# Performance work log

Measured on AMD Instinct MI355X. Metric: run time of the kernel, lower is better.

The kernel has to match this reference:

```python
import jax, jax.numpy as jnp
import numpy as np

ATTN_DIM = 1024
LATENT_DIM = 1024
N_HEADS = 16
HEAD_SIZE = ATTN_DIM // N_HEADS


def setup_inputs() -> dict:
    key = jax.random.key(0)
    ks = jax.random.split(key, 7)
    B, T = 2, 2048
    s_in = 1.0 / np.sqrt(LATENT_DIM)
    s_a = 1.0 / np.sqrt(ATTN_DIM)
    return {
        "x": jax.random.normal(ks[0], (B, T, LATENT_DIM), jnp.float32),
        "w_attn": jax.random.normal(ks[1], (LATENT_DIM, ATTN_DIM), jnp.float32) * s_in,
        "b_attn": jnp.zeros((ATTN_DIM,), jnp.float32),
        "w_qkv": jax.random.normal(ks[2], (ATTN_DIM, 3 * ATTN_DIM), jnp.float32) * s_a,
        "b_qkv": jnp.zeros((3 * ATTN_DIM,), jnp.float32),
        "w_proj": jax.random.normal(ks[3], (ATTN_DIM, ATTN_DIM), jnp.float32) * s_a,
        "b_proj": jnp.zeros((ATTN_DIM,), jnp.float32),
    }


def reference(x, w_attn, b_attn, w_qkv, b_qkv, w_proj, b_proj):
    # x: [B, T, latent_dim]
    h = jnp.einsum("btl,lc->btc", x, w_attn) + b_attn  # [B,T,C]
    B, T, C = h.shape
    qkv = jnp.einsum("btc,cd->btd", h, w_qkv) + b_qkv  # [B,T,3C]
    q, k, v = jnp.split(qkv, 3, axis=2)
    def heads(t):  # [B,T,C] -> [B,H,T,hs]
        return t.reshape(B, T, N_HEADS, HEAD_SIZE).transpose(0, 2, 1, 3)
    q, k, v = heads(q), heads(k), heads(v)
    scale = 1.0 / np.sqrt(HEAD_SIZE)
    scores = jnp.einsum("bhqd,bhkd->bhqk", q, k) * scale  # [B,H,T,T]
    attn = jax.nn.softmax(scores, axis=-1)
    out = jnp.einsum("bhqk,bhkd->bhqd", attn, v)  # [B,H,T,hs]
    out = out.transpose(0, 2, 1, 3).reshape(B, T, C)
    return jnp.einsum("btc,cd->btd", out, w_proj) + b_proj
```

## Files before the change

kernel.cpp:

```cpp
#include <hip/hip_runtime.h>

typedef unsigned short u16;
typedef unsigned int u32;
typedef __bf16 bf16x8 __attribute__((ext_vector_type(8)));
typedef float f32x4 __attribute__((ext_vector_type(4)));
typedef float f32x16 __attribute__((ext_vector_type(16)));
typedef unsigned uint2v __attribute__((ext_vector_type(2)));

typedef const __attribute__((address_space(1))) void* gcp_t;
typedef __attribute__((address_space(3))) void* lp_t;
#define GLDS16(g, l) __builtin_amdgcn_global_load_lds((gcp_t)(g), (lp_t)(l), 16, 0, 0)

__device__ __forceinline__ u16 f2bf(float f) {
  unsigned int u = __builtin_bit_cast(unsigned int, f);
  u += 0x7fffu + ((u >> 16) & 1u);
  return (u16)(u >> 16);
}
__device__ __forceinline__ u16 bfc(float f) {
  return __builtin_bit_cast(u16, (__bf16)f);
}
__device__ __forceinline__ u32 pkbf(float lo, float hi) {
  return (u32)bfc(lo) | ((u32)bfc(hi) << 16);
}
__device__ __forceinline__ float ex2(float x) {
  return __builtin_amdgcn_exp2f(x);
}

__global__ __launch_bounds__(256) void prep(const float* __restrict__ x, u16* __restrict__ xb,
                                            const float* __restrict__ wa, u16* __restrict__ wTa,
                                            const float* __restrict__ wq, u16* __restrict__ wTq,
                                            const float* __restrict__ wp, u16* __restrict__ wTp) {
  __shared__ float tile[32][33];
  const int idx = (int)blockIdx.x;
  const int tid = (int)threadIdx.x;
  if (idx < 2048) {
    long i = ((long)idx * 256 + tid) * 8;
    float4 a = *(const float4*)(x + i);
    float4 b = *(const float4*)(x + i + 4);
    union { u16 u[8]; int4 v; } pk;
    pk.u[0] = f2bf(a.x); pk.u[1] = f2bf(a.y); pk.u[2] = f2bf(a.z); pk.u[3] = f2bf(a.w);
    pk.u[4] = f2bf(b.x); pk.u[5] = f2bf(b.y); pk.u[6] = f2bf(b.z); pk.u[7] = f2bf(b.w);
    *(int4*)(xb + i) = pk.v;
    return;
  }
  const float* in; u16* out; int K, N, bx, by;
  if (idx < 3072) {
    int id = idx - 2048; in = wa; out = wTa; K = 1024; N = 1024; bx = id & 31; by = id >> 5;
  } else if (idx < 6144) {
    int id = idx - 3072; in = wq; out = wTq; K = 1024; N = 3072; bx = id % 96; by = id / 96;
  } else {
    int id = idx - 6144; in = wp; out = wTp; K = 1024; N = 1024; bx = id & 31; by = id >> 5;
  }
  const int n0 = bx * 32, k0 = by * 32;
  const int tx = tid & 31, ty = tid >> 5;
#pragma unroll
  for (int i = 0; i < 4; ++i)
    tile[ty + i * 8][tx] = in[(long)(k0 + ty + i * 8) * N + n0 + tx];
  __syncthreads();
#pragma unroll
  for (int i = 0; i < 4; ++i)
    out[(long)(n0 + ty + i * 8) * K + k0 + tx] = f2bf(tile[tx][ty + i * 8]);
}

template <int BM, int BN, int WN_WAVES, typename OutT, bool VSPLIT = false>
__global__ __launch_bounds__(256) void gemm_bt(const u16* __restrict__ A,
                                               const u16* __restrict__ Bt,
                                               const float* __restrict__ bias,
                                               OutT* __restrict__ C,
                                               u16* __restrict__ vout,
                                               int M, int N, int K) {
  constexpr int WM = BM / (4 / WN_WAVES);
  constexpr int WN = BN / WN_WAVES;
  constexpr int MF = WM / 16, NF = WN / 16;
  constexpr int STG = 2 * BM * 32 + 2 * BN * 32;
  constexpr int TRN = VSPLIT ? 128 * 136 : 0;
  constexpr int CEP = (sizeof(OutT) == 2) ? (BM * BN) : (2 * BM * BN);
  constexpr int PS1 = STG > TRN ? STG : TRN;
  constexpr int PSZ = PS1 > CEP ? PS1 : CEP;
  __shared__ __align__(16) u16 pool[PSZ];
  u16* lA0 = pool;
  u16* lB0 = pool + 2 * BM * 32;
  const int tid = (int)threadIdx.x;
  const int ln = tid & 63;
  const int w = tid >> 6;
  const int wr = w / WN_WAVES, wc = w % WN_WAVES;
  const int lr = ln & 15, lg = ln >> 4;

  const int nwg = (int)(gridDim.x * gridDim.y);
  const int lin = (int)(blockIdx.y * gridDim.x + blockIdx.x);
  const int cpx = nwg >> 3;
  const int swzb = (lin & 7) * cpx + (lin >> 3);
  const int bx = swzb % (int)gridDim.x;
  const int by = swzb / (int)gridDim.x;
  const long mBase = (long)by * BM;
  const long nBase = (long)bx * BN;

  f32x4 acc[MF][NF] = {};

  const int r0 = ln >> 2;
  const int c0 = (ln & 3) * 8;

  auto stage = [&](int buf, int k0) {
#pragma unroll
    for (int i = 0; i < BM / 64; ++i) {
      const int br = (i * 4 + w) * 16;
      GLDS16(A + (mBase + br + r0) * K + k0 + c0, lA0 + buf * BM * 32 + br * 32);
    }
#pragma unroll
    for (int i = 0; i < BN / 64; ++i) {
      const int br = (i * 4 + w) * 16;
      GLDS16(Bt + (nBase + br + r0) * K + k0 + c0, lB0 + buf * BN * 32 + br * 32);
    }
  };

  stage(0, 0);
  __syncthreads();
  int cur = 0;
  for (int k0 = 0; k0 < K; k0 += 32) {
    if (k0 + 32 < K) stage(cur ^ 1, k0 + 32);
    bf16x8 af[MF], bfv[NF];
#pragma unroll
    for (int mi = 0; mi < MF; ++mi)
      af[mi] = *(const bf16x8*)&lA0[cur * BM * 32 + (wr * WM + mi * 16 + lr) * 32 + lg * 8];
#pragma unroll
    for (int ni = 0; ni < NF; ++ni)
      bfv[ni] = *(const bf16x8*)&lB0[cur * BN * 32 + (wc * WN + ni * 16 + lr) * 32 + lg * 8];
#pragma unroll
    for (int mi = 0; mi < MF; ++mi)
#pragma unroll
      for (int ni = 0; ni < NF; ++ni)
        acc[mi][ni] = __builtin_amdgcn_mfma_f32_16x16x32_bf16(af[mi], bfv[ni],
                                                              acc[mi][ni], 0, 0, 0);
    __syncthreads();
    cur ^= 1;
  }

  if (VSPLIT && nBase >= 2048) {
#pragma unroll
    for (int ni = 0; ni < NF; ++ni) {
      const int cl = wc * WN + ni * 16 + lr;
      const float bv = bias ? bias[nBase + cl] : 0.f;
#pragma unroll
      for (int mi = 0; mi < MF; ++mi) {
#pragma unroll
        for (int j = 0; j < 4; ++j) {
          const int rl = wr * WM + mi * 16 + lg * 4 + j;
          pool[cl * 136 + rl] = bfc(acc[mi][ni][j] + bv);
        }
      }
    }
    __syncthreads();
    const int c = tid >> 1, half = tid & 1;
    const long cglob = nBase + c - 2048;
    const int hh2 = (int)(cglob >> 6), d = (int)(cglob & 63);
    const int bb = (int)(mBase >> 11);
    const int t0 = (int)(mBase & 2047);
    u16* dst = vout + ((long)(bb * 16 + hh2) * 64 + d) * 2048 + t0 + half * 64;
    const u16* srcp = &pool[c * 136 + half * 64];
#pragma unroll
    for (int i = 0; i < 8; ++i)
      *(int4*)(dst + i * 8) = *(const int4*)(srcp + i * 8);
    return;
  }

  if constexpr (sizeof(OutT) == 2) {
#pragma unroll
    for (int ni = 0; ni < NF; ++ni) {
      const int col = wc * WN + ni * 16 + lr;
      const float bv = bias ? bias[nBase + col] : 0.f;
#pragma unroll
      for (int mi = 0; mi < MF; ++mi)
#pragma unroll
        for (int j = 0; j < 4; ++j)
          pool[(wr * WM + mi * 16 + lg * 4 + j) * BN + col] = bfc(acc[mi][ni][j] + bv);
    }
    __syncthreads();
    constexpr int SL = BN / 8;
#pragma unroll
    for (int it = 0; it < BM * SL / 256; ++it) {
      const int S = it * 256 + tid;
      const int row = S / SL, si = S % SL;
      *(int4*)&C[(mBase + row) * N + nBase + si * 8] =
          *(const int4*)&pool[row * BN + si * 8];
    }
  } else {
    float* pf = (float*)pool;
#pragma unroll
    for (int ni = 0; ni < NF; ++ni) {
      const int col = wc * WN + ni * 16 + lr;
      const float bv = bias ? bias[nBase + col] : 0.f;
#pragma unroll
      for (int mi = 0; mi < MF; ++mi)
#pragma unroll
        for (int j = 0; j < 4; ++j)
          pf[(wr * WM + mi * 16 + lg * 4 + j) * BN + col] = acc[mi][ni][j] + bv;
    }
    __syncthreads();
    constexpr int SLF = BN / 4;
#pragma unroll
    for (int it = 0; it < BM * SLF / 256; ++it) {
      const int S = it * 256 + tid;
      const int row = S / SLF, si = S % SLF;
      *(f32x4*)&C[(mBase + row) * N + nBase + si * 4] =
          *(const f32x4*)&pf[row * BN + si * 4];
    }
  }
}

__global__ __launch_bounds__(512, 4) void attn_fwd(const u16* __restrict__ qkv,
                                                   const u16* __restrict__ vt,
                                                   u16* __restrict__ outp) {
  __shared__ __align__(16) u16 smem[2][2][2][64 * 64];
  const int tid = (int)threadIdx.x;
  const int ln = tid & 63;
  const int l31 = tid & 31;
  const int hiH = (tid >> 5) & 1;
  const int w = tid >> 6;
  const int g = w >> 2;
  const int qw = w & 3;
  const int bid0 = (int)blockIdx.x;
  const int bid = ((bid0 & 7) << 6) | (bid0 >> 3);
  const int qt = bid & 15;
  const int bh = bid >> 4;
  const int b = bh >> 4;
  const int hh = bh & 15;

  const float SCALE = 0.125f * 1.44269504088896f;

  const long qrow = (long)(b * 2048 + qt * 128 + qw * 32 + l31);
  const u16* Qp = qkv + qrow * 3072 + hh * 64;
  bf16x8 qf[4];
#pragma unroll
  for (int ks = 0; ks < 4; ++ks) {
    union { u16 u[8]; int4 i4; bf16x8 v; } in, ov;
    in.i4 = *(const int4*)(Qp + ks * 16 + hiH * 8);
#pragma unroll
    for (int e = 0; e < 8; ++e) {
      float f = __builtin_bit_cast(float, (u32)in.u[e] << 16) * SCALE;
      ov.u[e] = f2bf(f);
    }
    qf[ks] = ov.v;
  }

  f32x16 o[2] = {};
  float lsum = 0.f;

  const u16* Kbase = qkv + ((long)b * 2048) * 3072 + 1024 + hh * 64;
  const u16* Vbase = vt + (long)bh * 64 * 2048;

  const int sr = ln >> 3;
  const int scm = ln & 7;

  auto stageKV = [&](int buf, int t) {
    const int kv0 = (g * 16 + t) * 64;
#pragma unroll
    for (int i = 0; i < 2; ++i) {
      const int br = (i * 4 + qw) * 8;
      const int r = br + sr;
      const int cs = scm ^ (r & 7);
      GLDS16(Kbase + (long)(kv0 + r) * 3072 + cs * 8, &smem[g][buf][0][br * 64]);
      GLDS16(Vbase + (long)r * 2048 + kv0 + cs * 8, &smem[g][buf][1][br * 64]);
    }
  };

  stageKV(0, 0);
  __syncthreads();
  int cur = 0;
  for (int kt = 0; kt < 16; ++kt) {
    if (kt + 1 < 16) stageKV(cur ^ 1, kt + 1);
    const char* lK = (const char*)&smem[g][cur][0][0];
    const char* lV = (const char*)&smem[g][cur][1][0];

    f32x16 st[2] = {};
#pragma unroll
    for (int t = 0; t < 2; ++t) {
#pragma unroll
      for (int ks = 0; ks < 4; ++ks) {
        const int r = t * 32 + l31;
        int off = (r * 64 + ks * 16 + hiH * 8) * 2;
        off ^= (r & 7) << 4;
        const bf16x8 kf = *(const bf16x8*)(lK + off);
        st[t] = __builtin_amdgcn_mfma_f32_32x32x16_bf16(kf, qf[ks], st[t], 0, 0, 0);
      }
    }

#pragma unroll
    for (int t = 0; t < 2; ++t)
#pragma unroll
      for (int r = 0; r < 16; ++r) st[t][r] = ex2(st[t][r]);
    float ts[16];
#pragma unroll
    for (int r = 0; r < 16; ++r) ts[r] = st[0][r] + st[1][r];
#pragma unroll
    for (int s = 8; s > 0; s >>= 1)
#pragma unroll
      for (int r = 0; r < 8; ++r)
        if (r < s) ts[r] += ts[r + s];
    lsum += ts[0];

    bf16x8 pa[4];
#pragma unroll
    for (int t = 0; t < 2; ++t) {
#pragma unroll
      for (int gg = 0; gg < 2; ++gg) {
        const int bse = gg * 8;
        u32 A = pkbf(st[t][bse + 0], st[t][bse + 1]);
        u32 B = pkbf(st[t][bse + 2], st[t][bse + 3]);
        u32 C = pkbf(st[t][bse + 4], st[t][bse + 5]);
        u32 D = pkbf(st[t][bse + 6], st[t][bse + 7]);
        union { u32 wv[4]; bf16x8 v; } u;
#if __has_builtin(__builtin_amdgcn_permlane32_swap)
        uint2v r0 = __builtin_amdgcn_permlane32_swap(A, C, false, false);
        uint2v r1 = __builtin_amdgcn_permlane32_swap(B, D, false, false);
        u.wv[0] = r0[0]; u.wv[1] = r1[0]; u.wv[2] = r0[1]; u.wv[3] = r1[1];
#else
        const u32 sA = __shfl_xor((int)A, 32);
        const u32 sB = __shfl_xor((int)B, 32);
        const u32 sC = __shfl_xor((int)C, 32);
        const u32 sD = __shfl_xor((int)D, 32);
        u.wv[0] = hiH ? sC : A;
        u.wv[1] = hiH ? sD : B;
        u.wv[2] = hiH ? C : sA;
        u.wv[3] = hiH ? D : sB;
#endif
        pa[t * 2 + gg] = u.v;
      }
    }

#pragma unroll
    for (int dt = 0; dt < 2; ++dt) {
#pragma unroll
      for (int ks2 = 0; ks2 < 4; ++ks2) {
        const int r = dt * 32 + l31;
        int off = (r * 64 + ks2 * 16 + hiH * 8) * 2;
        off ^= (r & 7) << 4;
        const bf16x8 vf = *(const bf16x8*)(lV + off);
        o[dt] = __builtin_amdgcn_mfma_f32_32x32x16_bf16(vf, pa[ks2], o[dt], 0, 0, 0);
      }
    }
    __syncthreads();
    cur ^= 1;
  }

  const float lsum_tot = lsum + __shfl_xor(lsum, 32);
  float* PO = (float*)&smem[0][0][0][0];
  float* MLf = (float*)((char*)PO + 32768);

  if (g == 1) {
    float* dst = PO + (w - 4) * 2048 + ln * 32;
#pragma unroll
    for (int dt = 0; dt < 2; ++dt)
#pragma unroll
      for (int q4 = 0; q4 < 4; ++q4) {
        f32x4 c;
#pragma unroll
        for (int j = 0; j < 4; ++j) c[j] = o[dt][q4 * 4 + j];
        *(f32x4*)(dst + dt * 16 + q4 * 4) = c;
      }
    MLf[(w - 4) * 64 + ln] = lsum_tot;
  }
  __syncthreads();
  if (g == 0) {
    const float l1 = MLf[w * 64 + ln];
    const float* src = PO + w * 2048 + ln * 32;
    const float linv = 1.0f / (lsum_tot + l1);
    u16* T = (u16*)((char*)smem + 36864) + w * (32 * 72);
#pragma unroll
    for (int dt = 0; dt < 2; ++dt) {
      float o1[16];
#pragma unroll
      for (int q4 = 0; q4 < 4; ++q4) {
        const f32x4 c = *(const f32x4*)(src + dt * 16 + q4 * 4);
#pragma unroll
        for (int j = 0; j < 4; ++j) o1[q4 * 4 + j] = c[j];
      }
#pragma unroll
      for (int r = 0; r < 16; ++r) {
        const float v = (o[dt][r] + o1[r]) * linv;
        const int d = (r & 3) + 8 * (r >> 2) + 4 * hiH + dt * 32;
        T[l31 * 72 + d] = bfc(v);
      }
    }
    asm volatile("s_waitcnt lgkmcnt(0)" ::: "memory");
    __builtin_amdgcn_sched_barrier(0);
    const int rr = ln >> 1;
    const int c0 = (ln & 1) * 32;
    u16* orow = outp + ((long)(b * 2048 + qt * 128 + w * 32 + rr)) * 1024 + hh * 64 + c0;
#pragma unroll
    for (int i = 0; i < 4; ++i)
      *(int4*)(orow + i * 8) = *(const int4*)&T[rr * 72 + c0 + i * 8];
  }
}

extern "C" void kernel_launch(void* const* d_in, const int* in_sizes, int n_in,
                              void* d_out, int out_size, void* d_ws, size_t ws_size,
                              hipStream_t stream) {
  (void)in_sizes; (void)n_in; (void)out_size;
  const float* x = (const float*)d_in[0];
  const float* b_attn = (const float*)d_in[2];
  const float* b_qkv = (const float*)d_in[4];
  const float* b_proj = (const float*)d_in[6];

  char* ws = (char*)d_ws;
  const size_t MB = 1024 * 1024;
  u16* xb   = (u16*)(ws + 0 * MB);
  u16* hbuf = (u16*)(ws + 8 * MB);
  u16* qkvb = (u16*)(ws + 16 * MB);
  u16* vtb  = (u16*)(ws + 40 * MB);
  u16* aout = (u16*)(ws + 48 * MB);
  u16* wTa  = (u16*)(ws + 56 * MB);
  u16* wTq  = (u16*)(ws + 58 * MB);
  u16* wTp  = (u16*)(ws + 64 * MB);
  if (ws_size < 66 * MB) return;

  prep<<<7168, 256, 0, stream>>>(x, xb, (const float*)d_in[1], wTa,
                                 (const float*)d_in[3], wTq,
                                 (const float*)d_in[5], wTp);

  gemm_bt<64, 128, 4, u16><<<dim3(8, 64), 256, 0, stream>>>(
      xb, wTa, b_attn, hbuf, nullptr, 4096, 1024, 1024);
  gemm_bt<128, 128, 2, u16, true><<<dim3(24, 32), 256, 0, stream>>>(
      hbuf, wTq, b_qkv, qkvb, vtb, 4096, 3072, 1024);
  attn_fwd<<<512, 512, 0, stream>>>(qkvb, vtb, aout);
  gemm_bt<64, 128, 4, float><<<dim3(8, 64), 256, 0, stream>>>(
      aout, wTp, b_proj, (float*)d_out, nullptr, 4096, 1024, 1024);
}
```

Baseline: 130.2 us.

## Split attention KV range across four wave groups with 1024-thread blocks

Doubles the attention block to 1024 threads so four wave groups each process a quarter of the key/value sequence, instead of two groups each taking half. The double-buffered K/V staging becomes a single buffer that is loaded and then synchronised every tile. Partial outputs and row sums are combined in a two-round shared-memory reduction before normalisation. This adds waves to hide latency, but gives up the overlap of loads with compute and asks for 8 blocks per CU in the launch bounds, which may force register pressure or spills.

```diff
diff --git a/kernel.cpp b/kernel.cpp
--- a/kernel.cpp
+++ b/kernel.cpp
@@ -207,10 +207,11 @@
   }
 }
 
-__global__ __launch_bounds__(512, 4) void attn_fwd(const u16* __restrict__ qkv,
-                                                   const u16* __restrict__ vt,
-                                                   u16* __restrict__ outp) {
-  __shared__ __align__(16) u16 smem[2][2][2][64 * 64];
+__global__ __launch_bounds__(1024, 8) void attn_fwd(const u16* __restrict__ qkv,
+                                                    const u16* __restrict__ vt,
+                                                    u16* __restrict__ outp) {
+  __shared__ __align__(16) u16 smem[4][2][4096];
+  __shared__ float MLfA[256], MLfB[256];
   const int tid = (int)threadIdx.x;
   const int ln = tid & 63;
   const int l31 = tid & 31;
@@ -251,25 +252,23 @@
   const int sr = ln >> 3;
   const int scm = ln & 7;
 
-  auto stageKV = [&](int buf, int t) {
-    const int kv0 = (g * 16 + t) * 64;
+  auto stageKV = [&](int t) {
+    const int kv0 = g * 512 + t * 64;
 #pragma unroll
     for (int i = 0; i < 2; ++i) {
       const int br = (i * 4 + qw) * 8;
       const int r = br + sr;
       const int cs = scm ^ (r & 7);
-      GLDS16(Kbase + (long)(kv0 + r) * 3072 + cs * 8, &smem[g][buf][0][br * 64]);
-      GLDS16(Vbase + (long)r * 2048 + kv0 + cs * 8, &smem[g][buf][1][br * 64]);
+      GLDS16(Kbase + (long)(kv0 + r) * 3072 + cs * 8, &smem[g][0][br * 64]);
+      GLDS16(Vbase + (long)r * 2048 + kv0 + cs * 8, &smem[g][1][br * 64]);
     }
   };
 
-  stageKV(0, 0);
-  __syncthreads();
-  int cur = 0;
-  for (int kt = 0; kt < 16; ++kt) {
-    if (kt + 1 < 16) stageKV(cur ^ 1, kt + 1);
-    const char* lK = (const char*)&smem[g][cur][0][0];
-    const char* lV = (const char*)&smem[g][cur][1][0];
+  for (int kt = 0; kt < 8; ++kt) {
+    stageKV(kt);
+    __syncthreads();
+    const char* lK = (const char*)&smem[g][0][0];
+    const char* lV = (const char*)&smem[g][1][0];
 
     f32x16 st[2] = {};
 #pragma unroll
@@ -339,15 +338,13 @@
       }
     }
     __syncthreads();
-    cur ^= 1;
   }
 
   const float lsum_tot = lsum + __shfl_xor(lsum, 32);
-  float* PO = (float*)&smem[0][0][0][0];
-  float* MLf = (float*)((char*)PO + 32768);
-
-  if (g == 1) {
-    float* dst = PO + (w - 4) * 2048 + ln * 32;
+  float* PO = (float*)smem;
+
+  if (g == 1 || g == 3) {
+    float* dst = PO + (g == 3 ? 8192 : 0) + qw * 2048 + ln * 32;
 #pragma unroll
     for (int dt = 0; dt < 2; ++dt)
 #pragma unroll
@@ -357,35 +354,65 @@
         for (int j = 0; j < 4; ++j) c[j] = o[dt][q4 * 4 + j];
         *(f32x4*)(dst + dt * 16 + q4 * 4) = c;
       }
-    MLf[(w - 4) * 64 + ln] = lsum_tot;
+    if (g == 3) MLfB[qw * 64 + ln] = lsum_tot;
+    else        MLfA[qw * 64 + ln] = lsum_tot;
+  }
+  __syncthreads();
+  float lacc = lsum_tot;
+  if (g == 0 || g == 2) {
+    const float* src = PO + (g == 2 ? 8192 : 0) + qw * 2048 + ln * 32;
+    lacc += (g == 2 ? MLfB : MLfA)[qw * 64 + ln];
+#pragma unroll
+    for (int dt = 0; dt < 2; ++dt)
+#pragma unroll
+      for (int q4 = 0; q4 < 4; ++q4) {
+        const f32x4 c = *(const f32x4*)(src + dt * 16 + q4 * 4);
+#pragma unroll
+        for (int j = 0; j < 4; ++j) o[dt][q4 * 4 + j] += c[j];
+      }
+  }
+  __syncthreads();
+  if (g == 2) {
+    float* dst = PO + qw * 2048 + ln * 32;
+#pragma unroll
+    for (int dt = 0; dt < 2; ++dt)
+#pragma unroll
+      for (int q4 = 0; q4 < 4; ++q4) {
+        f32x4 c;
+#pragma unroll
+        for (int j = 0; j < 4; ++j) c[j] = o[dt][q4 * 4 + j];
+        *(f32x4*)(dst + dt * 16 + q4 * 4) = c;
+      }
+    MLfA[qw * 64 + ln] = lacc;
   }
   __syncthreads();
   if (g == 0) {
-    const float l1 = MLf[w * 64 + ln];
-    const float* src = PO + w * 2048 + ln * 32;
-    const float linv = 1.0f / (lsum_tot + l1);
-    u16* T = (u16*)((char*)smem + 36864) + w * (32 * 72);
-#pragma unroll
-    for (int dt = 0; dt < 2; ++dt) {
-      float o1[16];
+    const float* src = PO + qw * 2048 + ln * 32;
+    const float linv = 1.0f / (lacc + MLfA[qw * 64 + ln]);
+#pragma unroll
+    for (int dt = 0; dt < 2; ++dt)
 #pragma unroll
       for (int q4 = 0; q4 < 4; ++q4) {
         const f32x4 c = *(const f32x4*)(src + dt * 16 + q4 * 4);
 #pragma unroll
-        for (int j = 0; j < 4; ++j) o1[q4 * 4 + j] = c[j];
-      }
+        for (int j = 0; j < 4; ++j)
+          o[dt][q4 * 4 + j] = (o[dt][q4 * 4 + j] + c[j]) * linv;
+      }
+    asm volatile("" ::: "memory");
+    __builtin_amdgcn_sched_barrier(0);
+    u16* T = (u16*)smem + qw * 4096;
+#pragma unroll
+    for (int dt = 0; dt < 2; ++dt)
 #pragma unroll
       for (int r = 0; r < 16; ++r) {
-        const float v = (o[dt][r] + o1[r]) * linv;
         const int d = (r & 3) + 8 * (r >> 2) + 4 * hiH + dt * 32;
-        T[l31 * 72 + d] = bfc(v);
-      }
-    }
+        T[l31 * 72 + d] = bfc(o[dt][r]);
+      }
     asm volatile("s_waitcnt lgkmcnt(0)" ::: "memory");
     __builtin_amdgcn_sched_barrier(0);
     const int rr = ln >> 1;
     const int c0 = (ln & 1) * 32;
-    u16* orow = outp + ((long)(b * 2048 + qt * 128 + w * 32 + rr)) * 1024 + hh * 64 + c0;
+    u16* orow = outp + ((long)(b * 2048 + qt * 128 + qw * 32 + rr)) * 1024 + hh * 64 + c0;
 #pragma unroll
     for (int i = 0; i < 4; ++i)
       *(int4*)(orow + i * 8) = *(const int4*)&T[rr * 72 + c0 + i * 8];
@@ -421,7 +448,7 @@
       xb, wTa, b_attn, hbuf, nullptr, 4096, 1024, 1024);
   gemm_bt<128, 128, 2, u16, true><<<dim3(24, 32), 256, 0, stream>>>(
       hbuf, wTq, b_qkv, qkvb, vtb, 4096, 3072, 1024);
-  attn_fwd<<<512, 512, 0, stream>>>(qkvb, vtb, aout);
+  attn_fwd<<<512, 1024, 0, stream>>>(qkvb, vtb, aout);
   gemm_bt<64, 128, 4, float><<<dim3(8, 64), 256, 0, stream>>>(
       aout, wTp, b_proj, (float*)d_out, nullptr, 4096, 1024, 1024);
 }
```

New measurement: 330.2 us. 154% more time.
